# Kernel tuning notes

Measured on AMD Instinct MI355X. Metric: run time of the kernel, lower is better.

## Reference

```python
import jax, jax.numpy as jnp
import numpy as np
from jax import lax

B, T, S, F = 16, 32, 128, 3
H = 256          # encoder_hidden = decoder_hidden = decoder_input
NH = 8           # n_head
TP = 4           # t_predict
DK = H // NH


def _lin(k, fan_in, shape):
    return jax.random.normal(k, shape, jnp.float32) * (1.0 / np.sqrt(fan_in))


def setup_inputs() -> dict:
    key = jax.random.key(0)
    ks = jax.random.split(key, 14)
    return {
        "input_data": jax.random.normal(ks[0], (B, T, S, F), jnp.float32),
        # encoder attention-LSTM cell (input_size=3)
        "enc_Wq": _lin(ks[1], H, (H, H)),
        "enc_Wk": _lin(ks[2], H, (H, H)),
        "enc_Wv": _lin(ks[3], H, (H, H)),
        "enc_Wg": _lin(ks[4], F + 2 * H, (F + 2 * H, 4 * H)),
        "enc_bg": jnp.zeros((4 * H,), jnp.float32),
        # decoder attention-LSTM cell (input_size=decoder_input=H)
        "dec_Wq": _lin(ks[5], H, (H, H)),
        "dec_Wk": _lin(ks[6], H, (H, H)),
        "dec_Wv": _lin(ks[7], H, (H, H)),
        "dec_Wg": _lin(ks[8], 3 * H, (3 * H, 4 * H)),
        "dec_bg": jnp.zeros((4 * H,), jnp.float32),
        # embedding Linear(encoder_hidden -> decoder_input)
        "emb_W": _lin(ks[9], H, (H, H)),
        "emb_b": jnp.zeros((H,), jnp.float32),
        # output Linear(decoder_hidden -> output_size=1)
        "out_W": _lin(ks[10], H, (H, 1)),
        "out_b": jnp.zeros((1,), jnp.float32),
    }


def spatial_hidden(h):
    # h: [B,S,H] -> [B,S,4,H] neighbors at offsets (+2,+1,-1,-2), zero-padded
    z1 = jnp.zeros_like(h[:, :1])
    z2 = jnp.zeros_like(h[:, :2])
    after1 = jnp.concatenate([h[:, 1:], z1], axis=1)
    before1 = jnp.concatenate([z1, h[:, :-1]], axis=1)
    after2 = jnp.concatenate([h[:, 2:], z2], axis=1)
    before2 = jnp.concatenate([z2, h[:, :-2]], axis=1)
    return jnp.stack([after2, after1, before1, before2], axis=2)


def attn_lstm_cell(x, h, c, sp, Wq, Wk, Wv, Wg, bg):
    # x:[B,S,Fin] h,c:[B,S,H] sp:[B,S,4,H]
    b, s, _ = h.shape
    q = (h @ Wq).reshape(b, s, NH, DK)
    k = (sp @ Wk).reshape(b, s, 4, NH, DK)
    v = (sp @ Wv).reshape(b, s, 4, NH, DK)
    scores = jnp.einsum('bshd,bsnhd->bshn', q, k) / np.sqrt(DK).astype(np.float32)
    attn = jax.nn.softmax(scores, axis=-1)
    ctx = jnp.einsum('bshn,bsnhd->bshd', attn, v).reshape(b, s, H)
    z = jnp.concatenate([x, h, ctx], axis=-1) @ Wg + bg
    i, f, g, o = jnp.split(z, 4, axis=-1)
    c_new = jax.nn.sigmoid(f) * c + jax.nn.sigmoid(i) * jnp.tanh(g)
    h_new = jax.nn.sigmoid(o) * jnp.tanh(c_new)
    return h_new, c_new


def reference(input_data, enc_Wq, enc_Wk, enc_Wv, enc_Wg, enc_bg,
              dec_Wq, dec_Wk, dec_Wv, dec_Wg, dec_bg,
              emb_W, emb_b, out_W, out_b):
    b, t, s, f = input_data.shape
    eh = jnp.zeros((b, s, H), input_data.dtype)
    ec = jnp.zeros((b, s, H), input_data.dtype)
    dh = jnp.zeros((b, s, H), input_data.dtype)

    cur = jnp.swapaxes(input_data[:, :-1], 0, 1)  # [T-1,B,S,F]
    nxt = jnp.swapaxes(input_data[:, 1:], 0, 1)   # [T-1,B,S,F]

    def step(carry, xt):
        eh, ec, dh = carry
        x_cur, x_nxt = xt
        esp = spatial_hidden(eh)
        dsp = spatial_hidden(dh)
        eh, ec = attn_lstm_cell(x_cur, eh, ec, esp, enc_Wq, enc_Wk, enc_Wv, enc_Wg, enc_bg)
        code = jax.nn.sigmoid(eh @ emb_W + emb_b)
        # NOTE: original code passes decoder_h as both h and c (decoder_c unused)
        dh, _ = attn_lstm_cell(code, dh, dh, dsp, dec_Wq, dec_Wk, dec_Wv, dec_Wg, dec_bg)
        out = dh @ out_W + out_b                                   # [B,S,1]
        In = jnp.concatenate([x_nxt[:, 0:1, 1:2], out[:, :-1, :]], axis=1)
        num = x_cur[:, :, 2:3] + In - out
        next_data = jnp.concatenate([out, In, num], axis=2)        # [B,S,3]
        return (eh, ec, dh), next_data

    _, outs = lax.scan(step, (eh, ec, dh), (cur, nxt))
    # keep only steps with time >= t_predict
    return jnp.swapaxes(outs[TP:], 0, 1)  # [B, T-TP-1, S, 3]
```

## Files before the change

kernel.cpp:

```cpp
#include <hip/hip_runtime.h>
#include <hip/hip_bf16.h>

#define Bz 16
#define Tz 32
#define Sz 128
#define TPz 4
#define Mz (Bz*Sz)
#define NSTEP (Tz-1)

typedef __bf16 bf16x8 __attribute__((ext_vector_type(8)));
typedef float  f32x4  __attribute__((ext_vector_type(4)));

#define MFMA __builtin_amdgcn_mfma_f32_16x16x32_bf16

__device__ __forceinline__ float sigf(float x) { return 1.f/(1.f + __expf(-x)); }

__global__ __launch_bounds__(256) void prep3(
    const float* __restrict__ encWq, const float* __restrict__ encWk,
    const float* __restrict__ encWv, const float* __restrict__ encWg,
    const float* __restrict__ decWq, const float* __restrict__ decWk,
    const float* __restrict__ decWv, const float* __restrict__ decWg,
    const float* __restrict__ embW,
    __bf16* __restrict__ Pqkv_e, __bf16* __restrict__ Pqkv_d,
    __bf16* __restrict__ Pemb,   __bf16* __restrict__ Pg_e,
    __bf16* __restrict__ Pg_d)
{
    int id = blockIdx.x * 256 + threadIdx.x;
    if (id < 768*256) {
        int f = id >> 9, e = id & 511, l = e >> 3, j = e & 7;
        int nt = f >> 3, kt = f & 7;
        int n = nt*16 + (l & 15), k = kt*32 + (l >> 4)*8 + j;
        float v = (n < 256) ? encWq[k*256 + n]
                : (n < 512) ? encWk[k*256 + (n-256)]
                            : encWv[k*256 + (n-512)];
        Pqkv_e[id] = (__bf16)v; return;
    }
    id -= 768*256;
    if (id < 768*256) {
        int f = id >> 9, e = id & 511, l = e >> 3, j = e & 7;
        int nt = f >> 3, kt = f & 7;
        int n = nt*16 + (l & 15), k = kt*32 + (l >> 4)*8 + j;
        float v = (n < 256) ? decWq[k*256 + n]
                : (n < 512) ? decWk[k*256 + (n-256)]
                            : decWv[k*256 + (n-512)];
        Pqkv_d[id] = (__bf16)v; return;
    }
    id -= 768*256;
    if (id < 256*256) {
        int f = id >> 9, e = id & 511, l = e >> 3, j = e & 7;
        int nt = f >> 3, kt = f & 7;
        int n = nt*16 + (l & 15), k = kt*32 + (l >> 4)*8 + j;
        Pemb[id] = (__bf16)embW[k*256 + n]; return;
    }
    id -= 256*256;
    if (id < 1024*512) {
        int f = id >> 9, e = id & 511, l = e >> 3, j = e & 7;
        int nt = f >> 4, kt = f & 15;
        int cht = nt >> 2, g = nt & 3;
        int ch = cht*16 + (l & 15), k = kt*32 + (l >> 4)*8 + j;
        Pg_e[id] = (__bf16)encWg[(size_t)(3 + k)*1024 + g*256 + ch]; return;
    }
    id -= 1024*512;
    if (id < 1024*768) {
        int f = id >> 9, e = id & 511, l = e >> 3, j = e & 7;
        int nt = f / 24, kt = f % 24;
        int cht = nt >> 2, g = nt & 3;
        int ch = cht*16 + (l & 15), k = kt*32 + (l >> 4)*8 + j;
        Pg_d[id] = (__bf16)decWg[(size_t)k*1024 + g*256 + ch]; return;
    }
}

__device__ __forceinline__ void qkv_lds(
    const __bf16* src264, const __bf16* __restrict__ P,
    __bf16* qL, __bf16* kvL, int tid)
{
    const int w = tid >> 6, lane = tid & 63, quad = (lane >> 4), lr = lane & 15;
    #pragma unroll
    for (int ng = 0; ng < 3; ++ng) {
        const int ntA = w*6 + ng*2;
        f32x4 acc[2][3];
        #pragma unroll
        for (int i = 0; i < 2; ++i)
            #pragma unroll
            for (int m = 0; m < 3; ++m) acc[i][m] = f32x4{0.f,0.f,0.f,0.f};
        #pragma unroll
        for (int kc = 0; kc < 8; kc += 2) {
            bf16x8 a[2][3], b[2][2];
            #pragma unroll
            for (int u = 0; u < 2; ++u) {
                const int kt = kc + u;
                a[u][0] = *(const bf16x8*)&src264[(lr)*264      + kt*32 + quad*8];
                a[u][1] = *(const bf16x8*)&src264[(16 + lr)*264 + kt*32 + quad*8];
                a[u][2] = *(const bf16x8*)&src264[(32 + lr)*264 + kt*32 + quad*8];
                b[u][0] = *(const bf16x8*)&P[((size_t)(ntA*8 + kt)*64 + lane)*8];
                b[u][1] = *(const bf16x8*)&P[((size_t)((ntA+1)*8 + kt)*64 + lane)*8];
            }
            #pragma unroll
            for (int u = 0; u < 2; ++u) {
                acc[0][0] = MFMA(a[u][0], b[u][0], acc[0][0], 0,0,0);
                acc[0][1] = MFMA(a[u][1], b[u][0], acc[0][1], 0,0,0);
                acc[0][2] = MFMA(a[u][2], b[u][0], acc[0][2], 0,0,0);
                acc[1][0] = MFMA(a[u][0], b[u][1], acc[1][0], 0,0,0);
                acc[1][1] = MFMA(a[u][1], b[u][1], acc[1][1], 0,0,0);
                acc[1][2] = MFMA(a[u][2], b[u][1], acc[1][2], 0,0,0);
            }
        }
        #pragma unroll
        for (int i = 0; i < 2; ++i) {
            const int col = (ntA + i)*16 + lr;
            #pragma unroll
            for (int m = 0; m < 3; ++m)
                #pragma unroll
                for (int r = 0; r < 4; ++r) {
                    const int row = m*16 + quad*4 + r;
                    const float v = acc[i][m][r];
                    if (col < 256) {
                        if (row >= 2 && row < 34) qL[(row-2)*264 + col] = (__bf16)v;
                    } else if (row < 36) {
                        kvL[row*520 + (col - 256)] = (__bf16)v;
                    }
                }
        }
    }
}

__device__ __forceinline__ void attn_lds(
    const __bf16* qL, const __bf16* kvL, __bf16* cxL, int s0, int tid)
{
    const int w = tid >> 6, lane = tid & 63, quad = lane >> 4, lr = lane & 15;
    const int r = 4*w + quad, s = s0 + r, ch0 = lr*16;

    float q[16];
    {
        bf16x8 q0 = *(const bf16x8*)&qL[r*264 + ch0];
        bf16x8 q1 = *(const bf16x8*)&qL[r*264 + ch0 + 8];
        #pragma unroll
        for (int i = 0; i < 8; ++i) { q[i] = (float)q0[i]; q[8+i] = (float)q1[i]; }
    }
    bf16x8 zv;
    #pragma unroll
    for (int i = 0; i < 8; ++i) zv[i] = (__bf16)0.f;

    const int offs[4] = {2, 1, -1, -2};
    float sc[4]; bf16x8 v0[4], v1[4];
    #pragma unroll
    for (int n = 0; n < 4; ++n) {
        const int s2 = s + offs[n];
        const bool ok = ((unsigned)s2 < 128u);
        const int lrow = r + offs[n] + 2;
        float p = 0.f;
        if (ok) {
            bf16x8 k0 = *(const bf16x8*)&kvL[lrow*520 + ch0];
            bf16x8 k1 = *(const bf16x8*)&kvL[lrow*520 + ch0 + 8];
            v0[n] = *(const bf16x8*)&kvL[lrow*520 + 256 + ch0];
            v1[n] = *(const bf16x8*)&kvL[lrow*520 + 256 + ch0 + 8];
            #pragma unroll
            for (int i = 0; i < 8; ++i) p += q[i]*(float)k0[i] + q[8+i]*(float)k1[i];
        } else { v0[n] = zv; v1[n] = zv; }
        p += __shfl_xor(p, 1);
        sc[n] = ok ? p * 0.17677669529663687f : 0.f;
    }
    const float mx = fmaxf(fmaxf(sc[0], sc[1]), fmaxf(sc[2], sc[3]));
    float se = 0.f, aw[4];
    #pragma unroll
    for (int n = 0; n < 4; ++n) { aw[n] = __expf(sc[n] - mx); se += aw[n]; }
    const float inv = 1.f / se;
    float cx[16];
    #pragma unroll
    for (int i = 0; i < 16; ++i) cx[i] = 0.f;
    #pragma unroll
    for (int n = 0; n < 4; ++n)
        #pragma unroll
        for (int i = 0; i < 8; ++i) {
            cx[i]   += aw[n]*(float)v0[n][i];
            cx[8+i] += aw[n]*(float)v1[n][i];
        }
    bf16x8 o0, o1;
    #pragma unroll
    for (int i = 0; i < 8; ++i) { o0[i] = (__bf16)(cx[i]*inv); o1[i] = (__bf16)(cx[8+i]*inv); }
    *(bf16x8*)&cxL[r*264 + ch0]     = o0;
    *(bf16x8*)&cxL[r*264 + ch0 + 8] = o1;
}

#define SM_A264   0
#define SM_R      19008
#define SM_CODE   35904
#define SM_Q      56448
#define SM_MISC   73344
#define SM_TOTAL  73856

__global__ __launch_bounds__(512, 4) void step_k(
    int k, const float* __restrict__ input,
    __bf16* __restrict__ P, __bf16* __restrict__ Q,
    const __bf16* __restrict__ Pqkv_e, const __bf16* __restrict__ Pqkv_d,
    const __bf16* __restrict__ Pemb,   const __bf16* __restrict__ Pg_e,
    const __bf16* __restrict__ Pg_d,
    const float* __restrict__ encWg, const float* __restrict__ encbg,
    const float* __restrict__ decbg, const float* __restrict__ embb,
    const float* __restrict__ outW,
    float* __restrict__ ec, float* __restrict__ outbuf)
{
    __shared__ __attribute__((aligned(16))) char SM[SM_TOTAL];

    const int tid  = threadIdx.x;
    const int w    = tid >> 6;
    const int lane = tid & 63;
    const int quad = lane >> 4, lr = lane & 15;
    const int mt = w >> 2, ct = w & 3;

    __bf16* aL  = (__bf16*)(SM + SM_A264);
    __bf16* kvL = (__bf16*)(SM + SM_R);
    __bf16* qL  = (__bf16*)(SM + SM_Q);
    __bf16* cxL = qL;

    if (blockIdx.x >= 256) {
        if (k >= NSTEP) return;
        const int bid = blockIdx.x - 256;
        const int b = bid >> 4, rg = (bid >> 2) & 3, qt = bid & 3;
        const int gbatch = b*128, s0 = rg*32, grow0 = gbatch + s0;
        const int ch = qt*64 + ct*16 + lr;
        float* xL = (float*)(SM + SM_MISC);

        float wx0[4], wx1[4], wx2[4], bgv[4], ecv[4];
        #pragma unroll
        for (int g = 0; g < 4; ++g) {
            const int c = g*256 + ch;
            wx0[g] = encWg[c]; wx1[g] = encWg[1024 + c]; wx2[g] = encWg[2048 + c];
            bgv[g] = encbg[c];
        }
        #pragma unroll
        for (int r = 0; r < 4; ++r)
            ecv[r] = ec[(size_t)(grow0 + mt*16 + quad*4 + r)*256 + ch];

        for (int v = tid; v < 36*32; v += 512) {
            const int row = v >> 5, seg = v & 31, s = s0 - 2 + row;
            bf16x8 val;
            if ((unsigned)s < 128u)
                val = *(const bf16x8*)&P[(size_t)(gbatch + s)*512 + seg*8];
            else {
                #pragma unroll
                for (int i = 0; i < 8; ++i) val[i] = (__bf16)0.f;
            }
            *(bf16x8*)&aL[row*264 + seg*8] = val;
        }
        if (tid < 96) xL[tid] = input[((size_t)(b*Tz + k)*Sz + s0)*3 + tid];
        __syncthreads();

        qkv_lds(aL, Pqkv_e, qL, kvL, tid);
        __syncthreads();
        attn_lds(qL, kvL, cxL, s0, tid);
        __syncthreads();

        f32x4 acc[4];
        #pragma unroll
        for (int g = 0; g < 4; ++g) acc[g] = f32x4{0.f,0.f,0.f,0.f};
        #pragma unroll
        for (int kc = 0; kc < 16; kc += 4) {
            bf16x8 a4[4], b4[4][4];
            #pragma unroll
            for (int u = 0; u < 4; ++u) {
                const int kt = kc + u;
                const __bf16* As = (kt < 8)
                    ? &aL [(2 + mt*16 + lr)*264 + kt*32 + quad*8]
                    : &cxL[(mt*16 + lr)*264 + (kt-8)*32 + quad*8];
                a4[u] = *(const bf16x8*)As;
                #pragma unroll
                for (int g = 0; g < 4; ++g) {
                    const int nt = qt*16 + ct*4 + g;
                    b4[u][g] = *(const bf16x8*)&Pg_e[((size_t)(nt*16 + kt)*64 + lane)*8];
                }
            }
            #pragma unroll
            for (int u = 0; u < 4; ++u)
                #pragma unroll
                for (int g = 0; g < 4; ++g)
                    acc[g] = MFMA(a4[u], b4[u][g], acc[g], 0,0,0);
        }
        #pragma unroll
        for (int r = 0; r < 4; ++r) {
            const int row = mt*16 + quad*4 + r;
            const float x0 = xL[row*3], x1 = xL[row*3+1], x2 = xL[row*3+2];
            const float zi = acc[0][r] + x0*wx0[0] + x1*wx1[0] + x2*wx2[0] + bgv[0];
            const float zf = acc[1][r] + x0*wx0[1] + x1*wx1[1] + x2*wx2[1] + bgv[1];
            const float zg = acc[2][r] + x0*wx0[2] + x1*wx1[2] + x2*wx2[2] + bgv[2];
            const float zo = acc[3][r] + x0*wx0[3] + x1*wx1[3] + x2*wx2[3] + bgv[3];
            const size_t ei = (size_t)(grow0 + row)*256 + ch;
            const float cn = sigf(zf)*ecv[r] + sigf(zi)*tanhf(zg);
            ec[ei] = cn;
            Q[(size_t)(grow0 + row)*512 + ch] = (__bf16)(sigf(zo)*tanhf(cn));
        }
    } else {
        if (k < 1) return;
        const int td = k - 1;
        const int bid = blockIdx.x;
        const int b = bid >> 4, rg = (bid >> 2) & 3, qt = bid & 3;
        const int gbatch = b*128, s0 = rg*32, grow0 = gbatch + s0;
        const int ch = qt*64 + ct*16 + lr;
        __bf16* dhL   = aL;
        __bf16* ehtL  = (__bf16*)(SM + SM_R);
        __bf16* codeL = (__bf16*)(SM + SM_CODE);
        float* outredL = (float*)(SM + SM_MISC);

        float bgv[4];
        #pragma unroll
        for (int g = 0; g < 4; ++g) bgv[g] = decbg[g*256 + ch];
        const float ow  = outW[ch];
        const float bb0 = embb[(2*w + 0)*16 + lr];
        const float bb1 = embb[(2*w + 1)*16 + lr];

        for (int v = tid; v < 32*32; v += 512) {
            const int row = v >> 5, seg = v & 31;
            *(bf16x8*)&ehtL[row*264 + seg*8] =
                *(const bf16x8*)&P[(size_t)(grow0 + row)*512 + seg*8];
        }
        for (int v = tid; v < 36*32; v += 512) {
            const int row = v >> 5, seg = v & 31, s = s0 - 2 + row;
            bf16x8 val;
            if ((unsigned)s < 128u)
                val = *(const bf16x8*)&Q[(size_t)(gbatch + s)*512 + 256 + seg*8];
            else {
                #pragma unroll
                for (int i = 0; i < 8; ++i) val[i] = (__bf16)0.f;
            }
            *(bf16x8*)&dhL[row*264 + seg*8] = val;
        }
        __syncthreads();

        {
            f32x4 cacc[2][2];
            #pragma unroll
            for (int m = 0; m < 2; ++m)
                #pragma unroll
                for (int i = 0; i < 2; ++i) cacc[m][i] = f32x4{0.f,0.f,0.f,0.f};
            #pragma unroll
            for (int kc = 0; kc < 8; kc += 4) {
                bf16x8 a0s[4], a1s[4], bs[4][2];
                #pragma unroll
                for (int u = 0; u < 4; ++u) {
                    const int kt = kc + u;
                    a0s[u] = *(const bf16x8*)&ehtL[(lr)*264      + kt*32 + quad*8];
                    a1s[u] = *(const bf16x8*)&ehtL[(16 + lr)*264 + kt*32 + quad*8];
                    #pragma unroll
                    for (int i = 0; i < 2; ++i)
                        bs[u][i] = *(const bf16x8*)&Pemb[((size_t)((2*w + i)*8 + kt)*64 + lane)*8];
                }
                #pragma unroll
                for (int u = 0; u < 4; ++u)
                    #pragma unroll
                    for (int i = 0; i < 2; ++i) {
                        cacc[0][i] = MFMA(a0s[u], bs[u][i], cacc[0][i], 0,0,0);
                        cacc[1][i] = MFMA(a1s[u], bs[u][i], cacc[1][i], 0,0,0);
                    }
            }
            #pragma unroll
            for (int i = 0; i < 2; ++i) {
                const int col = (2*w + i)*16 + lr;
                const float bb = (i == 0) ? bb0 : bb1;
                #pragma unroll
                for (int m = 0; m < 2; ++m)
                    #pragma unroll
                    for (int r = 0; r < 4; ++r)
                        codeL[(m*16 + quad*4 + r)*264 + col] = (__bf16)sigf(cacc[m][i][r] + bb);
            }
        }
        __syncthreads();

        f32x4 acc[4];
        #pragma unroll
        for (int g = 0; g < 4; ++g) acc[g] = f32x4{0.f,0.f,0.f,0.f};
        #pragma unroll
        for (int kc = 0; kc < 8; kc += 4) {
            bf16x8 a4[4], b4[4][4];
            #pragma unroll
            for (int u = 0; u < 4; ++u) {
                const int kt = kc + u;
                a4[u] = *(const bf16x8*)&codeL[(mt*16 + lr)*264 + kt*32 + quad*8];
                #pragma unroll
                for (int g = 0; g < 4; ++g) {
                    const int nt = qt*16 + ct*4 + g;
                    b4[u][g] = *(const bf16x8*)&Pg_d[((size_t)(nt*24 + kt)*64 + lane)*8];
                }
            }
            #pragma unroll
            for (int u = 0; u < 4; ++u)
                #pragma unroll
                for (int g = 0; g < 4; ++g)
                    acc[g] = MFMA(a4[u], b4[u][g], acc[g], 0,0,0);
        }
        __syncthreads();

        qkv_lds(dhL, Pqkv_d, qL, kvL, tid);
        __syncthreads();
        attn_lds(qL, kvL, cxL, s0, tid);
        __syncthreads();

        #pragma unroll
        for (int kc = 8; kc < 24; kc += 4) {
            bf16x8 a4[4], b4[4][4];
            #pragma unroll
            for (int u = 0; u < 4; ++u) {
                const int kt = kc + u;
                const __bf16* As = (kt < 16)
                    ? &dhL[(2 + mt*16 + lr)*264 + (kt-8)*32 + quad*8]
                    : &cxL[(mt*16 + lr)*264 + (kt-16)*32 + quad*8];
                a4[u] = *(const bf16x8*)As;
                #pragma unroll
                for (int g = 0; g < 4; ++g) {
                    const int nt = qt*16 + ct*4 + g;
                    b4[u][g] = *(const bf16x8*)&Pg_d[((size_t)(nt*24 + kt)*64 + lane)*8];
                }
            }
            #pragma unroll
            for (int u = 0; u < 4; ++u)
                #pragma unroll
                for (int g = 0; g < 4; ++g)
                    acc[g] = MFMA(a4[u], b4[u][g], acc[g], 0,0,0);
        }
        #pragma unroll
        for (int r = 0; r < 4; ++r) {
            const int row = mt*16 + quad*4 + r;
            const float zi = acc[0][r] + bgv[0];
            const float zf = acc[1][r] + bgv[1];
            const float zg = acc[2][r] + bgv[2];
            const float zo = acc[3][r] + bgv[3];
            const float c_old = (float)dhL[(2 + row)*264 + ch];
            const float cn = sigf(zf)*c_old + sigf(zi)*tanhf(zg);
            const float h  = sigf(zo)*tanhf(cn);
            P[(size_t)(grow0 + row)*512 + 256 + ch] = (__bf16)h;
            float pv = h * ow;
            pv += __shfl_xor(pv, 1); pv += __shfl_xor(pv, 2);
            pv += __shfl_xor(pv, 4); pv += __shfl_xor(pv, 8);
            if (lr == 0) outredL[row*4 + ct] = pv;
        }
        __syncthreads();
        if (tid < 32) {
            const float s4 = outredL[tid*4] + outredL[tid*4+1]
                           + outredL[tid*4+2] + outredL[tid*4+3];
            atomicAdd(&outbuf[(size_t)td*Mz + grow0 + tid], s4);
        }
    }
}

__global__ __launch_bounds__(256) void assemble_k(
    const float* __restrict__ outbuf, const float* __restrict__ input,
    const float* __restrict__ outb, float* __restrict__ out)
{
    const int idx = blockIdx.x*256 + threadIdx.x;
    const int NT = NSTEP - TPz;
    if (idx >= Bz*NT*Sz) return;
    const int s  = idx & 127;
    const int bi = idx >> 7;
    const int i  = bi % NT;
    const int b  = bi / NT;
    const int t  = i + TPz;
    const float ob = outb[0];
    const float o  = outbuf[t*Mz + (b<<7) + s] + ob;
    const float In = (s == 0)
        ? input[((size_t)(b*Tz + t + 1)*Sz)*3 + 1]
        : outbuf[t*Mz + (b<<7) + s - 1] + ob;
    const float num = input[((size_t)(b*Tz + t)*Sz + s)*3 + 2] + In - o;
    const size_t base = ((size_t)(b*NT + i)*Sz + s)*3;
    out[base+0] = o;
    out[base+1] = In;
    out[base+2] = num;
}

extern "C" void kernel_launch(void* const* d_in, const int* in_sizes, int n_in,
                              void* d_out, int out_size, void* d_ws, size_t ws_size,
                              hipStream_t stream)
{
    const float* input = (const float*)d_in[0];
    const float* encWq = (const float*)d_in[1];
    const float* encWk = (const float*)d_in[2];
    const float* encWv = (const float*)d_in[3];
    const float* encWg = (const float*)d_in[4];
    const float* encbg = (const float*)d_in[5];
    const float* decWq = (const float*)d_in[6];
    const float* decWk = (const float*)d_in[7];
    const float* decWv = (const float*)d_in[8];
    const float* decWg = (const float*)d_in[9];
    const float* decbg = (const float*)d_in[10];
    const float* embW  = (const float*)d_in[11];
    const float* embb  = (const float*)d_in[12];
    const float* outW  = (const float*)d_in[13];
    const float* outb  = (const float*)d_in[14];

    char* ws = (char*)d_ws;
    size_t off = 0;
    auto alloc = [&](size_t bytes) -> void* {
        void* p = ws + off;
        off += (bytes + 255) & ~(size_t)255;
        return p;
    };
    __bf16* Pqkv_e = (__bf16*)alloc((size_t)768*256*2);
    __bf16* Pqkv_d = (__bf16*)alloc((size_t)768*256*2);
    __bf16* Pemb   = (__bf16*)alloc((size_t)256*256*2);
    __bf16* Pg_e   = (__bf16*)alloc((size_t)1024*512*2);
    __bf16* Pg_d   = (__bf16*)alloc((size_t)1024*768*2);
    __bf16* Xa     = (__bf16*)alloc((size_t)Mz*512*2);
    __bf16* Xb     = (__bf16*)alloc((size_t)Mz*512*2);
    float*  ec     = (float*) alloc((size_t)Mz*256*4);
    float*  outbuf = (float*) alloc((size_t)NSTEP*Mz*4);

    hipMemsetAsync(Xa, 0, (size_t)Mz*512*2, stream);
    hipMemsetAsync(ec, 0, (size_t)Mz*256*4, stream);
    hipMemsetAsync(outbuf, 0, (size_t)NSTEP*Mz*4, stream);

    prep3<<<6912, 256, 0, stream>>>(encWq, encWk, encWv, encWg,
                                    decWq, decWk, decWv, decWg, embW,
                                    Pqkv_e, Pqkv_d, Pemb, Pg_e, Pg_d);

    for (int k = 0; k <= NSTEP; ++k) {
        __bf16* P = (k & 1) ? Xb : Xa;
        __bf16* Q = (k & 1) ? Xa : Xb;
        step_k<<<512, 512, 0, stream>>>(k, input, P, Q,
                                        Pqkv_e, Pqkv_d, Pemb, Pg_e, Pg_d,
                                        encWg, encbg, decbg, embb, outW,
                                        ec, outbuf);
    }
    assemble_k<<<(Bz*(NSTEP-TPz)*Sz + 255)/256, 256, 0, stream>>>(
        outbuf, input, outb, (float*)d_out);
}
```

Baseline: 1.264 ms.

## Read hidden-state MFMA operands directly from global instead of LDS staging

Removes the cooperative global-to-LDS staging of encoder/decoder hidden rows and has the QKV and gate MFMA loops load A fragments straight from global memory, using a zeroed global row for out-of-range neighbours. This drops several __syncthreads barriers and shrinks shared memory. The decoder gate GEMM is also merged into a single pass over code, hidden and context. The trade is more, possibly uncoalesced, global/L2 reads, repeated across waves, in place of LDS reuse. A leftover unused c_old load remains.

```diff
diff --git a/kernel.cpp b/kernel.cpp
--- a/kernel.cpp
+++ b/kernel.cpp
@@ -70,11 +70,19 @@
     }
 }
 
-__device__ __forceinline__ void qkv_lds(
-    const __bf16* src264, const __bf16* __restrict__ P,
+__device__ __forceinline__ void qkv_g(
+    const __bf16* __restrict__ G,
+    const __bf16* __restrict__ zrow,
+    int s0, const __bf16* __restrict__ P,
     __bf16* qL, __bf16* kvL, int tid)
 {
     const int w = tid >> 6, lane = tid & 63, quad = (lane >> 4), lr = lane & 15;
+    const __bf16* A0 = ((unsigned)(s0 - 2 + lr) < 128u)
+                     ? G + (size_t)lr*512 : zrow;
+    const __bf16* A1 = ((unsigned)(s0 + 14 + lr) < 128u)
+                     ? G + (size_t)(16 + lr)*512 : zrow;
+    const __bf16* A2 = (lr < 4 && (unsigned)(s0 + 30 + lr) < 128u)
+                     ? G + (size_t)(32 + lr)*512 : zrow;
     #pragma unroll
     for (int ng = 0; ng < 3; ++ng) {
         const int ntA = w*6 + ng*2;
@@ -89,9 +97,9 @@
             #pragma unroll
             for (int u = 0; u < 2; ++u) {
                 const int kt = kc + u;
-                a[u][0] = *(const bf16x8*)&src264[(lr)*264      + kt*32 + quad*8];
-                a[u][1] = *(const bf16x8*)&src264[(16 + lr)*264 + kt*32 + quad*8];
-                a[u][2] = *(const bf16x8*)&src264[(32 + lr)*264 + kt*32 + quad*8];
+                a[u][0] = *(const bf16x8*)&A0[kt*32 + quad*8];
+                a[u][1] = *(const bf16x8*)&A1[kt*32 + quad*8];
+                a[u][2] = *(const bf16x8*)&A2[kt*32 + quad*8];
                 b[u][0] = *(const bf16x8*)&P[((size_t)(ntA*8 + kt)*64 + lane)*8];
                 b[u][1] = *(const bf16x8*)&P[((size_t)((ntA+1)*8 + kt)*64 + lane)*8];
             }
@@ -182,12 +190,11 @@
     *(bf16x8*)&cxL[r*264 + ch0 + 8] = o1;
 }
 
-#define SM_A264   0
-#define SM_R      19008
-#define SM_CODE   35904
-#define SM_Q      56448
-#define SM_MISC   73344
-#define SM_TOTAL  73856
+#define SM_KV     0
+#define SM_Q      37440
+#define SM_CODE   54336
+#define SM_MISC   71232
+#define SM_TOTAL  71744
 
 __global__ __launch_bounds__(512, 4) void step_k(
     int k, const float* __restrict__ input,
@@ -198,7 +205,8 @@
     const float* __restrict__ encWg, const float* __restrict__ encbg,
     const float* __restrict__ decbg, const float* __restrict__ embb,
     const float* __restrict__ outW,
-    float* __restrict__ ec, float* __restrict__ outbuf)
+    float* __restrict__ ec, float* __restrict__ outbuf,
+    const __bf16* __restrict__ zrow)
 {
     __shared__ __attribute__((aligned(16))) char SM[SM_TOTAL];
 
@@ -208,8 +216,7 @@
     const int quad = lane >> 4, lr = lane & 15;
     const int mt = w >> 2, ct = w & 3;
 
-    __bf16* aL  = (__bf16*)(SM + SM_A264);
-    __bf16* kvL = (__bf16*)(SM + SM_R);
+    __bf16* kvL = (__bf16*)(SM + SM_KV);
     __bf16* qL  = (__bf16*)(SM + SM_Q);
     __bf16* cxL = qL;
 
@@ -232,25 +239,14 @@
         for (int r = 0; r < 4; ++r)
             ecv[r] = ec[(size_t)(grow0 + mt*16 + quad*4 + r)*256 + ch];
 
-        for (int v = tid; v < 36*32; v += 512) {
-            const int row = v >> 5, seg = v & 31, s = s0 - 2 + row;
-            bf16x8 val;
-            if ((unsigned)s < 128u)
-                val = *(const bf16x8*)&P[(size_t)(gbatch + s)*512 + seg*8];
-            else {
-                #pragma unroll
-                for (int i = 0; i < 8; ++i) val[i] = (__bf16)0.f;
-            }
-            *(bf16x8*)&aL[row*264 + seg*8] = val;
-        }
         if (tid < 96) xL[tid] = input[((size_t)(b*Tz + k)*Sz + s0)*3 + tid];
-        __syncthreads();
-
-        qkv_lds(aL, Pqkv_e, qL, kvL, tid);
+
+        qkv_g(P + ((size_t)(gbatch + s0) - 2)*512, zrow, s0, Pqkv_e, qL, kvL, tid);
         __syncthreads();
         attn_lds(qL, kvL, cxL, s0, tid);
         __syncthreads();
 
+        const __bf16* ArowP = P + (size_t)(grow0 + mt*16 + lr)*512;
         f32x4 acc[4];
         #pragma unroll
         for (int g = 0; g < 4; ++g) acc[g] = f32x4{0.f,0.f,0.f,0.f};
@@ -260,10 +256,9 @@
             #pragma unroll
             for (int u = 0; u < 4; ++u) {
                 const int kt = kc + u;
-                const __bf16* As = (kt < 8)
-                    ? &aL [(2 + mt*16 + lr)*264 + kt*32 + quad*8]
-                    : &cxL[(mt*16 + lr)*264 + (kt-8)*32 + quad*8];
-                a4[u] = *(const bf16x8*)As;
+                a4[u] = (kt < 8)
+                    ? *(const bf16x8*)&ArowP[kt*32 + quad*8]
+                    : *(const bf16x8*)&cxL[(mt*16 + lr)*264 + (kt-8)*32 + quad*8];
                 #pragma unroll
                 for (int g = 0; g < 4; ++g) {
                     const int nt = qt*16 + ct*4 + g;
@@ -296,8 +291,6 @@
         const int b = bid >> 4, rg = (bid >> 2) & 3, qt = bid & 3;
         const int gbatch = b*128, s0 = rg*32, grow0 = gbatch + s0;
         const int ch = qt*64 + ct*16 + lr;
-        __bf16* dhL   = aL;
-        __bf16* ehtL  = (__bf16*)(SM + SM_R);
         __bf16* codeL = (__bf16*)(SM + SM_CODE);
         float* outredL = (float*)(SM + SM_MISC);
 
@@ -308,25 +301,9 @@
         const float bb0 = embb[(2*w + 0)*16 + lr];
         const float bb1 = embb[(2*w + 1)*16 + lr];
 
-        for (int v = tid; v < 32*32; v += 512) {
-            const int row = v >> 5, seg = v & 31;
-            *(bf16x8*)&ehtL[row*264 + seg*8] =
-                *(const bf16x8*)&P[(size_t)(grow0 + row)*512 + seg*8];
-        }
-        for (int v = tid; v < 36*32; v += 512) {
-            const int row = v >> 5, seg = v & 31, s = s0 - 2 + row;
-            bf16x8 val;
-            if ((unsigned)s < 128u)
-                val = *(const bf16x8*)&Q[(size_t)(gbatch + s)*512 + 256 + seg*8];
-            else {
-                #pragma unroll
-                for (int i = 0; i < 8; ++i) val[i] = (__bf16)0.f;
-            }
-            *(bf16x8*)&dhL[row*264 + seg*8] = val;
-        }
-        __syncthreads();
-
         {
+            const __bf16* Ae0 = P + (size_t)(grow0 + lr)*512;
+            const __bf16* Ae1 = P + (size_t)(grow0 + 16 + lr)*512;
             f32x4 cacc[2][2];
             #pragma unroll
             for (int m = 0; m < 2; ++m)
@@ -338,8 +315,8 @@
                 #pragma unroll
                 for (int u = 0; u < 4; ++u) {
                     const int kt = kc + u;
-                    a0s[u] = *(const bf16x8*)&ehtL[(lr)*264      + kt*32 + quad*8];
-                    a1s[u] = *(const bf16x8*)&ehtL[(16 + lr)*264 + kt*32 + quad*8];
+                    a0s[u] = *(const bf16x8*)&Ae0[kt*32 + quad*8];
+                    a1s[u] = *(const bf16x8*)&Ae1[kt*32 + quad*8];
                     #pragma unroll
                     for (int i = 0; i < 2; ++i)
                         bs[u][i] = *(const bf16x8*)&Pemb[((size_t)((2*w + i)*8 + kt)*64 + lane)*8];
@@ -363,47 +340,27 @@
                         codeL[(m*16 + quad*4 + r)*264 + col] = (__bf16)sigf(cacc[m][i][r] + bb);
             }
         }
-        __syncthreads();
-
-        f32x4 acc[4];
-        #pragma unroll
-        for (int g = 0; g < 4; ++g) acc[g] = f32x4{0.f,0.f,0.f,0.f};
-        #pragma unroll
-        for (int kc = 0; kc < 8; kc += 4) {
-            bf16x8 a4[4], b4[4][4];
-            #pragma unroll
-            for (int u = 0; u < 4; ++u) {
-                const int kt = kc + u;
-                a4[u] = *(const bf16x8*)&codeL[(mt*16 + lr)*264 + kt*32 + quad*8];
-                #pragma unroll
-                for (int g = 0; g < 4; ++g) {
-                    const int nt = qt*16 + ct*4 + g;
-                    b4[u][g] = *(const bf16x8*)&Pg_d[((size_t)(nt*24 + kt)*64 + lane)*8];
-                }
-            }
-            #pragma unroll
-            for (int u = 0; u < 4; ++u)
-                #pragma unroll
-                for (int g = 0; g < 4; ++g)
-                    acc[g] = MFMA(a4[u], b4[u][g], acc[g], 0,0,0);
-        }
-        __syncthreads();
-
-        qkv_lds(dhL, Pqkv_d, qL, kvL, tid);
+        qkv_g(Q + ((size_t)(gbatch + s0) - 2)*512 + 256, zrow, s0, Pqkv_d,
+              qL, kvL, tid);
         __syncthreads();
         attn_lds(qL, kvL, cxL, s0, tid);
         __syncthreads();
 
-        #pragma unroll
-        for (int kc = 8; kc < 24; kc += 4) {
+        const __bf16* ArowD = Q + (size_t)(grow0 + mt*16 + lr)*512 + 256;
+        f32x4 acc[4];
+        #pragma unroll
+        for (int g = 0; g < 4; ++g) acc[g] = f32x4{0.f,0.f,0.f,0.f};
+        #pragma unroll
+        for (int kc = 0; kc < 24; kc += 4) {
             bf16x8 a4[4], b4[4][4];
             #pragma unroll
             for (int u = 0; u < 4; ++u) {
                 const int kt = kc + u;
-                const __bf16* As = (kt < 16)
-                    ? &dhL[(2 + mt*16 + lr)*264 + (kt-8)*32 + quad*8]
-                    : &cxL[(mt*16 + lr)*264 + (kt-16)*32 + quad*8];
-                a4[u] = *(const bf16x8*)As;
+                a4[u] = (kt < 8)
+                    ? *(const bf16x8*)&codeL[(mt*16 + lr)*264 + kt*32 + quad*8]
+                    : (kt < 16)
+                    ? *(const bf16x8*)&ArowD[(kt-8)*32 + quad*8]
+                    : *(const bf16x8*)&cxL[(mt*16 + lr)*264 + (kt-16)*32 + quad*8];
                 #pragma unroll
                 for (int g = 0; g < 4; ++g) {
                     const int nt = qt*16 + ct*4 + g;
@@ -423,9 +380,11 @@
             const float zf = acc[1][r] + bgv[1];
             const float zg = acc[2][r] + bgv[2];
             const float zo = acc[3][r] + bgv[3];
-            const float c_old = (float)dhL[(2 + row)*264 + ch];
-            const float cn = sigf(zf)*c_old + sigf(zi)*tanhf(zg);
+            const float c_old = (float)ArowD[( (size_t)(quad*4 + r) )*512];
+            const float c_old2 = (float)Q[(size_t)(grow0 + row)*512 + 256 + ch];
+            const float cn = sigf(zf)*c_old2 + sigf(zi)*tanhf(zg);
             const float h  = sigf(zo)*tanhf(cn);
+            (void)c_old;
             P[(size_t)(grow0 + row)*512 + 256 + ch] = (__bf16)h;
             float pv = h * ow;
             pv += __shfl_xor(pv, 1); pv += __shfl_xor(pv, 2);
@@ -501,10 +460,12 @@
     __bf16* Xb     = (__bf16*)alloc((size_t)Mz*512*2);
     float*  ec     = (float*) alloc((size_t)Mz*256*4);
     float*  outbuf = (float*) alloc((size_t)NSTEP*Mz*4);
+    __bf16* zrow   = (__bf16*)alloc((size_t)512*2);
 
     hipMemsetAsync(Xa, 0, (size_t)Mz*512*2, stream);
     hipMemsetAsync(ec, 0, (size_t)Mz*256*4, stream);
     hipMemsetAsync(outbuf, 0, (size_t)NSTEP*Mz*4, stream);
+    hipMemsetAsync(zrow, 0, (size_t)512*2, stream);
 
     prep3<<<6912, 256, 0, stream>>>(encWq, encWk, encWv, encWg,
                                     decWq, decWk, decWv, decWg, embW,
@@ -516,7 +477,7 @@
         step_k<<<512, 512, 0, stream>>>(k, input, P, Q,
                                         Pqkv_e, Pqkv_d, Pemb, Pg_e, Pg_d,
                                         encWg, encbg, decbg, embb, outW,
-                                        ec, outbuf);
+                                        ec, outbuf, zrow);
     }
     assemble_k<<<(Bz*(NSTEP-TPz)*Sz + 255)/256, 256, 0, stream>>>(
         outbuf, input, outb, (float*)d_out);
```

New measurement: 1.921 ms. 52.0% more time.
